# Kernel optimization log

Measured on AMD Instinct MI355X. Metric: run time of the kernel, lower is better.

Reference implementation:

```python
import jax, jax.numpy as jnp
import numpy as np

DEPTH = 4
N_MOLS = 2000
ATOMS_PER_MOL = 50
N_ATOMS = N_MOLS * ATOMS_PER_MOL + 1   # +1 zero-padding row (chemprop convention)
N_BONDS = 200001                        # +1 zero-padding row
MAX_NB = 6
ATOM_FDIM, BOND_FDIM, HIDDEN = 133, 147, 300


def setup_inputs() -> dict:
    key = jax.random.key(0)
    ks = jax.random.split(key, 12)
    f_atoms = jax.random.uniform(ks[0], (N_ATOMS, ATOM_FDIM), jnp.float32).at[0].set(0.0)
    f_bonds = jax.random.uniform(ks[1], (N_BONDS, BOND_FDIM), jnp.float32).at[0].set(0.0)
    w_atoms = jax.random.uniform(ks[2], (N_ATOMS,), jnp.float32) + 0.5
    w_bonds = (jax.random.uniform(ks[3], (N_BONDS,), jnp.float32) + 0.5).at[0].set(0.0)
    a2b = jax.random.randint(ks[4], (N_ATOMS, MAX_NB), 0, N_BONDS, jnp.int32)
    b2a = jax.random.randint(ks[5], (N_BONDS,), 0, N_ATOMS, jnp.int32)
    b2revb = jax.random.randint(ks[6], (N_BONDS,), 0, N_BONDS, jnp.int32)
    # segment id per atom; padding atom 0 -> dummy segment N_MOLS (dropped)
    mol_id = jnp.concatenate([jnp.array([N_MOLS], jnp.int32),
                              jnp.repeat(jnp.arange(N_MOLS, dtype=jnp.int32), ATOMS_PER_MOL)])
    degree_of_polym = jax.random.uniform(ks[7], (N_MOLS,), jnp.float32) + 0.5
    s = 0.05
    W_i = jax.random.normal(ks[8], (BOND_FDIM, HIDDEN), jnp.float32) * s
    W_h = jax.random.normal(ks[9], (HIDDEN, HIDDEN), jnp.float32) * s
    W_o = jax.random.normal(ks[10], (ATOM_FDIM + HIDDEN, HIDDEN), jnp.float32) * s
    b_o = jnp.zeros((HIDDEN,), jnp.float32)
    return dict(f_atoms=f_atoms, f_bonds=f_bonds, w_atoms=w_atoms, w_bonds=w_bonds,
                degree_of_polym=degree_of_polym, W_i=W_i, W_h=W_h, W_o=W_o, b_o=b_o,
                a2b=a2b, b2a=b2a, b2revb=b2revb, mol_id=mol_id)


def reference(f_atoms, f_bonds, w_atoms, w_bonds, degree_of_polym,
              W_i, W_h, W_o, b_o, a2b, b2a, b2revb, mol_id):
    # bond-message MPNN (atom_messages=False, undirected=False, ReLU, dropout=0 eval)
    inp = f_bonds @ W_i                                   # [n_bonds, H], no bias
    message = jax.nn.relu(inp)
    for _ in range(DEPTH - 1):
        # gather incoming directed-bond messages per atom and weight them
        nei_msg = message[a2b] * w_bonds[a2b][..., None]  # [n_atoms, max_nb, H]
        a_message = nei_msg.sum(axis=1)                   # [n_atoms, H]
        # subtract reverse message (weighted)
        message = a_message[b2a] - message[b2revb] * w_bonds[:, None]
        message = jax.nn.relu(inp + message @ W_h)
    # final atom aggregation
    nei_msg = message[a2b] * w_bonds[a2b][..., None]
    a_message = nei_msg.sum(axis=1)                       # [n_atoms, H]
    a_input = jnp.concatenate([f_atoms, a_message], axis=1)
    atom_hiddens = jax.nn.relu(a_input @ W_o + b_o)       # [n_atoms, H]
    # per-molecule weighted mean readout, scaled by degree of polymerization
    weighted = w_atoms[:, None] * atom_hiddens
    sums = jax.ops.segment_sum(weighted, mol_id, num_segments=N_MOLS + 1)[:N_MOLS]
    wsum = jax.ops.segment_sum(w_atoms, mol_id, num_segments=N_MOLS + 1)[:N_MOLS]
    mol_vecs = degree_of_polym[:, None] * (sums / wsum[:, None])
    return mol_vecs
```

## Files before the change

### kernel.cpp

```cpp
#include <hip/hip_runtime.h>

#define N_MOLS  2000
#define APM     50
#define N_ATOMS 100001
#define N_BONDS 200001
#define MAX_NB  6
#define AF      133
#define BF      147
#define H       300

#define SB    320
#define SF    160
#define MB_P  200192
#define MA_P  100096
#define SWH   320
#define SWI   160
#define SWO   480

typedef _Float16 f16x8 __attribute__((ext_vector_type(8)));
typedef _Float16 f16x4 __attribute__((ext_vector_type(4)));
typedef float    f32x4 __attribute__((ext_vector_type(4)));
typedef float    f32x2 __attribute__((ext_vector_type(2)));

__device__ inline void fp8x8_dec(const uint2 u, float* f) {
    const f32x2 d0 = __builtin_amdgcn_cvt_pk_f32_fp8(u.x, false);
    const f32x2 d1 = __builtin_amdgcn_cvt_pk_f32_fp8(u.x, true);
    const f32x2 d2 = __builtin_amdgcn_cvt_pk_f32_fp8(u.y, false);
    const f32x2 d3 = __builtin_amdgcn_cvt_pk_f32_fp8(u.y, true);
    f[0]=d0[0]; f[1]=d0[1]; f[2]=d1[0]; f[3]=d1[1];
    f[4]=d2[0]; f[5]=d2[1]; f[6]=d3[0]; f[7]=d3[1];
}
__device__ inline uint2 fp8x8_enc(const float* f) {
    int w0 = __builtin_amdgcn_cvt_pk_fp8_f32(f[0], f[1], 0, false);
    w0 = __builtin_amdgcn_cvt_pk_fp8_f32(f[2], f[3], w0, true);
    int w1 = __builtin_amdgcn_cvt_pk_fp8_f32(f[4], f[5], 0, false);
    w1 = __builtin_amdgcn_cvt_pk_fp8_f32(f[6], f[7], w1, true);
    uint2 r; r.x = (unsigned)w0; r.y = (unsigned)w1; return r;
}

__global__ void cast_fb_kernel(const float* __restrict__ src, _Float16* __restrict__ dst) {
    unsigned i = blockIdx.x * blockDim.x + threadIdx.x;
    if (i >= (unsigned)MB_P * SF) return;
    unsigned m = i / SF, k = i % SF;
    dst[i] = (_Float16)((m < N_BONDS && k < BF) ? src[(size_t)m * BF + k] : 0.f);
}
__global__ void cast_fa_kernel(const float* __restrict__ src, _Float16* __restrict__ dst) {
    unsigned i = blockIdx.x * blockDim.x + threadIdx.x;
    if (i >= (unsigned)MA_P * SF) return;
    unsigned m = i / SF, k = i % SF;
    dst[i] = (_Float16)((m < N_ATOMS && k < AF) ? src[(size_t)m * AF + k] : 0.f);
}
__global__ void cast_wh_kernel(const float* __restrict__ W, _Float16* __restrict__ Wt) {
    int i = blockIdx.x * blockDim.x + threadIdx.x;
    if (i >= 320 * SWH) return;
    const int e = i & 7, quad = (i >> 3) & 3, r16 = (i >> 5) & 15;
    const int rest = i >> 9, ctg = rest % 20, kc = rest / 20;
    const int n = ctg * 16 + r16, k = kc * 32 + quad * 8 + e;
    Wt[i] = (_Float16)((n < H && k < H) ? W[k * H + n] : 0.f);
}
__global__ void cast_wi_kernel(const float* __restrict__ W, _Float16* __restrict__ Wt) {
    int i = blockIdx.x * blockDim.x + threadIdx.x;
    if (i >= 320 * SWI) return;
    const int e = i & 7, quad = (i >> 3) & 3, r16 = (i >> 5) & 15;
    const int rest = i >> 9, ctg = rest % 20, kc = rest / 20;
    const int n = ctg * 16 + r16, k = kc * 32 + quad * 8 + e;
    Wt[i] = (_Float16)((n < H && k < BF) ? W[k * H + n] : 0.f);
}
__global__ void cast_wo_kernel(const float* __restrict__ W, _Float16* __restrict__ Wt) {
    int i = blockIdx.x * blockDim.x + threadIdx.x;
    if (i >= 320 * SWO) return;
    const int e = i & 7, quad = (i >> 3) & 3, r16 = (i >> 5) & 15;
    const int rest = i >> 9, ctg = rest % 20, kc = rest / 20;
    const int n = ctg * 16 + r16, k = kc * 32 + quad * 8 + e;
    float v = 0.f;
    if (n < H) {
        if (k < 320) { if (k < H) v = W[(AF + k) * H + n]; }
        else         { int rr = k - 320; if (rr < AF) v = W[rr * H + n]; }
    }
    Wt[i] = (_Float16)v;
}

template<int NCHUNK, int MODE>
__global__ __launch_bounds__(256, 2) void dgemm_kernel(
    const _Float16* __restrict__ A1, const _Float16* __restrict__ A2,
    const unsigned char* __restrict__ A8,
    const _Float16* __restrict__ Wt, const float* __restrict__ bias,
    _Float16* __restrict__ out16, unsigned char* __restrict__ out8)
{
    __shared__ __align__(16) _Float16 stage[32 * 324];

    const int tid  = threadIdx.x;
    const int lane = tid & 63, wave = tid >> 6;
    const int r16  = lane & 15, quad = lane >> 4;
    const int rowhalf = wave >> 1, colhalf = wave & 1;
    const int row0 = blockIdx.x * 128 + rowhalf * 64;
    const int colb = colhalf * 160;

    f32x4 acc[4][10];
    #pragma unroll
    for (int s = 0; s < 4; ++s)
        #pragma unroll
        for (int ct = 0; ct < 10; ++ct) acc[s][ct] = f32x4{0.f, 0.f, 0.f, 0.f};

    const _Float16* wb = Wt + (size_t)colhalf * 10 * 512 + (r16 * 4 + quad) * 8;

    #pragma unroll
    for (int kc = 0; kc < NCHUNK; ++kc) {
        f16x8 a[4];
        if constexpr (MODE == 4 || MODE == 5) {
            #pragma unroll
            for (int s = 0; s < 4; ++s) {
                const uint2 u = *(const uint2*)(A8 + (size_t)(row0 + s * 16 + r16) * 320 + kc * 32 + quad * 8);
                float f[8];
                fp8x8_dec(u, f);
                #pragma unroll
                for (int j = 0; j < 8; ++j) {
                    float v = f[j];
                    if (MODE == 4) v = v > 0.f ? v : 0.f;
                    a[s][j] = (_Float16)v;
                }
            }
        } else {
            const _Float16* ap; int kl, sa;
            if (MODE == 2 && kc >= 10) { ap = A2; kl = kc - 10; sa = SF; }
            else                       { ap = A1; kl = kc; sa = (MODE == 0 ? SF : SB); }
            #pragma unroll
            for (int s = 0; s < 4; ++s)
                a[s] = *(const f16x8*)(ap + (size_t)(row0 + s * 16 + r16) * sa + kl * 32 + quad * 8);
        }
        #pragma unroll
        for (int ct = 0; ct < 10; ++ct) {
            const f16x8 b = *(const f16x8*)(wb + (size_t)(kc * 20 + ct) * 512);
            #pragma unroll
            for (int s = 0; s < 4; ++s)
                acc[s][ct] = __builtin_amdgcn_mfma_f32_16x16x32_f16(a[s], b, acc[s][ct], 0, 0, 0);
        }
    }

    #pragma unroll
    for (int p = 0; p < 4; ++p) {
        if ((p >> 1) == rowhalf) {
            const int sb0 = (p & 1) * 2;
            #pragma unroll
            for (int s2 = 0; s2 < 2; ++s2) {
                const int s = sb0 + s2;
                #pragma unroll
                for (int ct = 0; ct < 10; ++ct) {
                    const int col = colb + ct * 16 + r16;
                    const float bv = (MODE == 2 && col < H) ? bias[col] : 0.f;
                    const int lr = s2 * 16 + quad * 4;
                    #pragma unroll
                    for (int e = 0; e < 4; ++e)
                        stage[(lr + e) * 324 + col] = (_Float16)(acc[s][ct][e] + bv);
                }
            }
        }
        __syncthreads();
        #pragma unroll
        for (int i = 0; i < 5; ++i) {
            const int c = tid + i * 256;
            const int row = c / 40, colc = (c % 40) * 8;
            const _Float16* sp = stage + row * 324 + colc;
            const f16x4 vlo = *(const f16x4*)(sp);
            const f16x4 vhi = *(const f16x4*)(sp + 4);
            f16x8 v;
            #pragma unroll
            for (int j = 0; j < 4; ++j) { v[j] = vlo[j]; v[j + 4] = vhi[j]; }
            const size_t off = (size_t)(blockIdx.x * 128 + p * 32 + row) * SB + colc;
            if (MODE == 0) {
                float f[8];
                #pragma unroll
                for (int j = 0; j < 8; ++j) f[j] = (float)v[j];
                *(uint2*)(out8 + off) = fp8x8_enc(f);
            } else {
                if (MODE == 2) {
                    #pragma unroll
                    for (int j = 0; j < 8; ++j)
                        v[j] = (v[j] > (_Float16)0) ? v[j] : (_Float16)0;
                }
                *(f16x8*)(out16 + off) = v;
            }
        }
        if (p < 3) __syncthreads();
    }
}

__global__ __launch_bounds__(256, 8) void aggregate_kernel(
    const _Float16* __restrict__ src,
    const int* __restrict__ a2b,
    const float* __restrict__ w_bonds,
    _Float16* __restrict__ dst)
{
    const int lane = threadIdx.x & 63;
    const int a = blockIdx.x * 4 + (threadIdx.x >> 6);
    if (a >= N_ATOMS || lane >= 40) return;
    const int h0 = lane * 8;
    float acc[8] = {0, 0, 0, 0, 0, 0, 0, 0};
    #pragma unroll
    for (int k = 0; k < MAX_NB; ++k) {
        const int b = a2b[a * MAX_NB + k];
        const float w = w_bonds[b];
        const f16x8 m = *(const f16x8*)(src + (size_t)b * SB + h0);
        #pragma unroll
        for (int j = 0; j < 8; ++j) acc[j] += w * (float)m[j];
    }
    f16x8 o;
    #pragma unroll
    for (int j = 0; j < 8; ++j) o[j] = (_Float16)acc[j];
    *(f16x8*)(dst + (size_t)a * SB + h0) = o;
}

__global__ __launch_bounds__(256, 8) void aggregate8_kernel(
    const unsigned char* __restrict__ src,
    const int* __restrict__ a2b,
    const float* __restrict__ w_bonds,
    _Float16* __restrict__ dst)
{
    const int lane = threadIdx.x & 63;
    const int a = blockIdx.x * 4 + (threadIdx.x >> 6);
    if (a >= N_ATOMS || lane >= 40) return;
    const int h0 = lane * 8;
    float acc[8] = {0, 0, 0, 0, 0, 0, 0, 0};
    #pragma unroll
    for (int k = 0; k < MAX_NB; ++k) {
        const int b = a2b[a * MAX_NB + k];
        const float w = w_bonds[b];
        const uint2 u = *(const uint2*)(src + (size_t)b * 320 + h0);
        float f[8];
        fp8x8_dec(u, f);
        #pragma unroll
        for (int j = 0; j < 8; ++j) acc[j] += w * f[j];
    }
    f16x8 o;
    #pragma unroll
    for (int j = 0; j < 8; ++j) o[j] = (_Float16)acc[j];
    *(f16x8*)(dst + (size_t)a * SB + h0) = o;
}

__global__ __launch_bounds__(256, 8) void update_kernel(
    const unsigned char* __restrict__ inp8,
    const _Float16* __restrict__ hm,
    const _Float16* __restrict__ hb,
    const int* __restrict__ b2a,
    const int* __restrict__ b2revb,
    const float* __restrict__ w_bonds,
    unsigned char* __restrict__ msg8)
{
    const int lane = threadIdx.x & 63;
    const int b = blockIdx.x * 4 + (threadIdx.x >> 6);
    if (b >= MB_P || lane >= 40) return;
    const bool real = b < N_BONDS;
    const int bc = real ? b : 0;
    const int a  = b2a[bc];
    const int rb = b2revb[bc];
    const float w = w_bonds[bc];
    const int h0 = lane * 8;
    const uint2 i8  = *(const uint2*)(inp8 + (size_t)b * 320 + h0);
    const f16x8 hmv = *(const f16x8*)(hm + (size_t)a  * SB + h0);
    const f16x8 hbv = *(const f16x8*)(hb + (size_t)rb * SB + h0);
    float inpf[8];
    fp8x8_dec(i8, inpf);
    float o[8];
    #pragma unroll
    for (int j = 0; j < 8; ++j) {
        const float v = inpf[j] + (float)hmv[j] - w * (float)hbv[j];
        o[j] = (real && v > 0.f) ? v : 0.f;
    }
    *(uint2*)(msg8 + (size_t)b * 320 + h0) = fp8x8_enc(o);
}

__global__ __launch_bounds__(256, 8) void readout_kernel(
    const _Float16* __restrict__ ah,
    const float* __restrict__ w_atoms,
    const float* __restrict__ dop,
    float* __restrict__ out)
{
    const int lane = threadIdx.x & 63;
    const int m = blockIdx.x * 4 + (threadIdx.x >> 6);
    if (m >= N_MOLS || lane >= 40) return;
    const int h0 = lane * 8;
    const int a0 = 1 + m * APM;
    float acc[8] = {0, 0, 0, 0, 0, 0, 0, 0};
    float wsum = 0.f;
    for (int i = 0; i < APM; ++i) {
        const float w = w_atoms[a0 + i];
        wsum += w;
        const f16x8 v = *(const f16x8*)(ah + (size_t)(a0 + i) * SB + h0);
        #pragma unroll
        for (int j = 0; j < 8; ++j) acc[j] += w * (float)v[j];
    }
    const float s = dop[m] / wsum;
    #pragma unroll
    for (int j = 0; j < 8; ++j) {
        const int h = h0 + j;
        if (h < H) out[(size_t)m * H + h] = s * acc[j];
    }
}

extern "C" void kernel_launch(void* const* d_in, const int* in_sizes, int n_in,
                              void* d_out, int out_size, void* d_ws, size_t ws_size,
                              hipStream_t stream) {
    const float* f_atoms = (const float*)d_in[0];
    const float* f_bonds = (const float*)d_in[1];
    const float* w_atoms = (const float*)d_in[2];
    const float* w_bonds = (const float*)d_in[3];
    const float* dop     = (const float*)d_in[4];
    const float* W_i     = (const float*)d_in[5];
    const float* W_h     = (const float*)d_in[6];
    const float* W_o     = (const float*)d_in[7];
    const float* b_o     = (const float*)d_in[8];
    const int* a2b    = (const int*)d_in[9];
    const int* b2a    = (const int*)d_in[10];
    const int* b2revb = (const int*)d_in[11];
    float* out = (float*)d_out;

    char* p = (char*)d_ws;
    auto alloc = [&](size_t bytes) {
        char* q = p;
        p += ((bytes + 64 + 255) / 256) * 256;
        return q;
    };
    unsigned char* inp8 = (unsigned char*)alloc((size_t)MB_P * 320);
    unsigned char* msg8 = (unsigned char*)alloc((size_t)MB_P * 320);
    _Float16* hb   = (_Float16*)alloc((size_t)MB_P * SB * 2);
    _Float16* hm   = (_Float16*)alloc((size_t)MA_P * SB * 2);
    _Float16* Wth  = (_Float16*)alloc((size_t)320 * SWH * 2);
    _Float16* Wti  = (_Float16*)alloc((size_t)320 * SWI * 2);
    _Float16* Wto  = (_Float16*)alloc((size_t)320 * SWO * 2);
    _Float16* fb16 = hb;
    _Float16* fa16 = (_Float16*)inp8;
    _Float16* ah   = hb;

    if ((size_t)(p - (char*)d_ws) > ws_size) {
        hipMemsetAsync(d_out, 0, (size_t)out_size * sizeof(float), stream);
        return;
    }

    {
        unsigned n1 = (unsigned)MB_P * SF;
        cast_fb_kernel<<<(n1 + 255) / 256, 256, 0, stream>>>(f_bonds, fb16);
        cast_wh_kernel<<<(320 * SWH + 255) / 256, 256, 0, stream>>>(W_h, Wth);
        cast_wi_kernel<<<(320 * SWI + 255) / 256, 256, 0, stream>>>(W_i, Wti);
        cast_wo_kernel<<<(320 * SWO + 255) / 256, 256, 0, stream>>>(W_o, Wto);
    }

    const int gB = MB_P / 128;
    const int gA = MA_P / 128;
    const int aggGrid = (N_ATOMS + 3) / 4;
    const int updGrid = MB_P / 4;

    dgemm_kernel<5, 0><<<gB, 256, 0, stream>>>(fb16, nullptr, nullptr, Wti, nullptr, nullptr, inp8);
    dgemm_kernel<10, 4><<<gB, 256, 0, stream>>>(nullptr, nullptr, inp8, Wth, nullptr, hb, nullptr);
    aggregate_kernel<<<aggGrid, 256, 0, stream>>>(hb, a2b, w_bonds, hm);
    update_kernel<<<updGrid, 256, 0, stream>>>(inp8, hm, hb, b2a, b2revb, w_bonds, msg8);
    dgemm_kernel<10, 5><<<gB, 256, 0, stream>>>(nullptr, nullptr, msg8, Wth, nullptr, hb, nullptr);
    aggregate_kernel<<<aggGrid, 256, 0, stream>>>(hb, a2b, w_bonds, hm);
    update_kernel<<<updGrid, 256, 0, stream>>>(inp8, hm, hb, b2a, b2revb, w_bonds, msg8);
    dgemm_kernel<10, 5><<<gB, 256, 0, stream>>>(nullptr, nullptr, msg8, Wth, nullptr, hb, nullptr);
    aggregate_kernel<<<aggGrid, 256, 0, stream>>>(hb, a2b, w_bonds, hm);
    update_kernel<<<updGrid, 256, 0, stream>>>(inp8, hm, hb, b2a, b2revb, w_bonds, msg8);
    aggregate8_kernel<<<aggGrid, 256, 0, stream>>>(msg8, a2b, w_bonds, hm);
    {
        unsigned n2 = (unsigned)MA_P * SF;
        cast_fa_kernel<<<(n2 + 255) / 256, 256, 0, stream>>>(f_atoms, fa16);
    }
    dgemm_kernel<15, 2><<<gA, 256, 0, stream>>>(hm, fa16, nullptr, Wto, b_o, ah, nullptr);
    readout_kernel<<<(N_MOLS + 3) / 4, 256, 0, stream>>>(ah, w_atoms, dop, out);
}
```

Measured before the change: 1.137 ms.

## Stage fp8 A tiles through LDS and pack elementwise threads densely

Adds a dedicated fp8-input GEMM kernel that copies the block's 128x320 fp8 A tile into shared memory with coalesced 16-byte loads, then decodes from LDS, replacing strided 8-byte global loads per lane. The aggregate and update kernels switch from one wave per row with 24 idle lanes to flat indexing over row×40 chunks, so every lane does work. The generic GEMM now always applies ReLU on fp16 output, since only MODE 2 still uses it. The cost is extra LDS use (about 42KB per block) that may limit occupancy, plus div/mod by 40 in the elementwise kernels.

```diff
diff --git a/kernel.cpp b/kernel.cpp
--- a/kernel.cpp
+++ b/kernel.cpp
@@ -83,7 +83,6 @@
 template<int NCHUNK, int MODE>
 __global__ __launch_bounds__(256, 2) void dgemm_kernel(
     const _Float16* __restrict__ A1, const _Float16* __restrict__ A2,
-    const unsigned char* __restrict__ A8,
     const _Float16* __restrict__ Wt, const float* __restrict__ bias,
     _Float16* __restrict__ out16, unsigned char* __restrict__ out8)
 {
@@ -106,28 +105,13 @@
 
     #pragma unroll
     for (int kc = 0; kc < NCHUNK; ++kc) {
+        const _Float16* ap; int kl, sa;
+        if (MODE == 2 && kc >= 10) { ap = A2; kl = kc - 10; sa = SF; }
+        else                       { ap = A1; kl = kc; sa = (MODE == 0 ? SF : SB); }
         f16x8 a[4];
-        if constexpr (MODE == 4 || MODE == 5) {
-            #pragma unroll
-            for (int s = 0; s < 4; ++s) {
-                const uint2 u = *(const uint2*)(A8 + (size_t)(row0 + s * 16 + r16) * 320 + kc * 32 + quad * 8);
-                float f[8];
-                fp8x8_dec(u, f);
-                #pragma unroll
-                for (int j = 0; j < 8; ++j) {
-                    float v = f[j];
-                    if (MODE == 4) v = v > 0.f ? v : 0.f;
-                    a[s][j] = (_Float16)v;
-                }
-            }
-        } else {
-            const _Float16* ap; int kl, sa;
-            if (MODE == 2 && kc >= 10) { ap = A2; kl = kc - 10; sa = SF; }
-            else                       { ap = A1; kl = kc; sa = (MODE == 0 ? SF : SB); }
-            #pragma unroll
-            for (int s = 0; s < 4; ++s)
-                a[s] = *(const f16x8*)(ap + (size_t)(row0 + s * 16 + r16) * sa + kl * 32 + quad * 8);
-        }
+        #pragma unroll
+        for (int s = 0; s < 4; ++s)
+            a[s] = *(const f16x8*)(ap + (size_t)(row0 + s * 16 + r16) * sa + kl * 32 + quad * 8);
         #pragma unroll
         for (int ct = 0; ct < 10; ++ct) {
             const f16x8 b = *(const f16x8*)(wb + (size_t)(kc * 20 + ct) * 512);
@@ -173,13 +157,103 @@
                 for (int j = 0; j < 8; ++j) f[j] = (float)v[j];
                 *(uint2*)(out8 + off) = fp8x8_enc(f);
             } else {
-                if (MODE == 2) {
-                    #pragma unroll
-                    for (int j = 0; j < 8; ++j)
-                        v[j] = (v[j] > (_Float16)0) ? v[j] : (_Float16)0;
-                }
+                #pragma unroll
+                for (int j = 0; j < 8; ++j)
+                    v[j] = (v[j] > (_Float16)0) ? v[j] : (_Float16)0;
                 *(f16x8*)(out16 + off) = v;
             }
+        }
+        if (p < 3) __syncthreads();
+    }
+}
+
+template<int RELU>
+__global__ __launch_bounds__(256, 2) void dgemm8_kernel(
+    const unsigned char* __restrict__ A8,
+    const _Float16* __restrict__ Wt,
+    _Float16* __restrict__ out16)
+{
+    __shared__ __align__(16) unsigned char Als[128 * 328];
+    __shared__ __align__(16) _Float16 stage[32 * 324];
+
+    const int tid  = threadIdx.x;
+    const int lane = tid & 63, wave = tid >> 6;
+    const int r16  = lane & 15, quad = lane >> 4;
+    const int rowhalf = wave >> 1, colhalf = wave & 1;
+    const int colb = colhalf * 160;
+    const size_t gbase = (size_t)blockIdx.x * 128 * 320;
+
+    #pragma unroll
+    for (int i = 0; i < 10; ++i) {
+        const int idx = tid + i * 256;
+        const int row = idx / 20, col = idx % 20;
+        const uint4 v = *(const uint4*)(A8 + gbase + (size_t)idx * 16);
+        *(uint4*)(&Als[row * 328 + col * 16]) = v;
+    }
+    __syncthreads();
+
+    f32x4 acc[4][10];
+    #pragma unroll
+    for (int s = 0; s < 4; ++s)
+        #pragma unroll
+        for (int ct = 0; ct < 10; ++ct) acc[s][ct] = f32x4{0.f, 0.f, 0.f, 0.f};
+
+    const _Float16* wb = Wt + (size_t)colhalf * 10 * 512 + (r16 * 4 + quad) * 8;
+
+    #pragma unroll
+    for (int kc = 0; kc < 10; ++kc) {
+        f16x8 a[4];
+        #pragma unroll
+        for (int s = 0; s < 4; ++s) {
+            const int lrow = rowhalf * 64 + s * 16 + r16;
+            const uint2 u = *(const uint2*)(&Als[lrow * 328 + kc * 32 + quad * 8]);
+            float f[8];
+            fp8x8_dec(u, f);
+            #pragma unroll
+            for (int j = 0; j < 8; ++j) {
+                float v = f[j];
+                if (RELU) v = v > 0.f ? v : 0.f;
+                a[s][j] = (_Float16)v;
+            }
+        }
+        #pragma unroll
+        for (int ct = 0; ct < 10; ++ct) {
+            const f16x8 b = *(const f16x8*)(wb + (size_t)(kc * 20 + ct) * 512);
+            #pragma unroll
+            for (int s = 0; s < 4; ++s)
+                acc[s][ct] = __builtin_amdgcn_mfma_f32_16x16x32_f16(a[s], b, acc[s][ct], 0, 0, 0);
+        }
+    }
+
+    #pragma unroll
+    for (int p = 0; p < 4; ++p) {
+        if ((p >> 1) == rowhalf) {
+            const int sb0 = (p & 1) * 2;
+            #pragma unroll
+            for (int s2 = 0; s2 < 2; ++s2) {
+                const int s = sb0 + s2;
+                #pragma unroll
+                for (int ct = 0; ct < 10; ++ct) {
+                    const int col = colb + ct * 16 + r16;
+                    const int lr = s2 * 16 + quad * 4;
+                    #pragma unroll
+                    for (int e = 0; e < 4; ++e)
+                        stage[(lr + e) * 324 + col] = (_Float16)acc[s][ct][e];
+                }
+            }
+        }
+        __syncthreads();
+        #pragma unroll
+        for (int i = 0; i < 5; ++i) {
+            const int c = tid + i * 256;
+            const int row = c / 40, colc = (c % 40) * 8;
+            const _Float16* sp = stage + row * 324 + colc;
+            const f16x4 vlo = *(const f16x4*)(sp);
+            const f16x4 vhi = *(const f16x4*)(sp + 4);
+            f16x8 v;
+            #pragma unroll
+            for (int j = 0; j < 4; ++j) { v[j] = vlo[j]; v[j + 4] = vhi[j]; }
+            *(f16x8*)(out16 + (size_t)(blockIdx.x * 128 + p * 32 + row) * SB + colc) = v;
         }
         if (p < 3) __syncthreads();
     }
@@ -191,10 +265,10 @@
     const float* __restrict__ w_bonds,
     _Float16* __restrict__ dst)
 {
-    const int lane = threadIdx.x & 63;
-    const int a = blockIdx.x * 4 + (threadIdx.x >> 6);
-    if (a >= N_ATOMS || lane >= 40) return;
-    const int h0 = lane * 8;
+    const unsigned idx = blockIdx.x * 256 + threadIdx.x;
+    if (idx >= (unsigned)N_ATOMS * 40) return;
+    const int a = idx / 40, c = idx % 40;
+    const int h0 = c * 8;
     float acc[8] = {0, 0, 0, 0, 0, 0, 0, 0};
     #pragma unroll
     for (int k = 0; k < MAX_NB; ++k) {
@@ -216,10 +290,10 @@
     const float* __restrict__ w_bonds,
     _Float16* __restrict__ dst)
 {
-    const int lane = threadIdx.x & 63;
-    const int a = blockIdx.x * 4 + (threadIdx.x >> 6);
-    if (a >= N_ATOMS || lane >= 40) return;
-    const int h0 = lane * 8;
+    const unsigned idx = blockIdx.x * 256 + threadIdx.x;
+    if (idx >= (unsigned)N_ATOMS * 40) return;
+    const int a = idx / 40, c = idx % 40;
+    const int h0 = c * 8;
     float acc[8] = {0, 0, 0, 0, 0, 0, 0, 0};
     #pragma unroll
     for (int k = 0; k < MAX_NB; ++k) {
@@ -246,15 +320,15 @@
     const float* __restrict__ w_bonds,
     unsigned char* __restrict__ msg8)
 {
-    const int lane = threadIdx.x & 63;
-    const int b = blockIdx.x * 4 + (threadIdx.x >> 6);
-    if (b >= MB_P || lane >= 40) return;
+    const unsigned idx = blockIdx.x * 256 + threadIdx.x;
+    if (idx >= (unsigned)MB_P * 40) return;
+    const int b = idx / 40, c = idx % 40;
     const bool real = b < N_BONDS;
     const int bc = real ? b : 0;
     const int a  = b2a[bc];
     const int rb = b2revb[bc];
     const float w = w_bonds[bc];
-    const int h0 = lane * 8;
+    const int h0 = c * 8;
     const uint2 i8  = *(const uint2*)(inp8 + (size_t)b * 320 + h0);
     const f16x8 hmv = *(const f16x8*)(hm + (size_t)a  * SB + h0);
     const f16x8 hbv = *(const f16x8*)(hb + (size_t)rb * SB + h0);
@@ -346,17 +420,17 @@
 
     const int gB = MB_P / 128;
     const int gA = MA_P / 128;
-    const int aggGrid = (N_ATOMS + 3) / 4;
-    const int updGrid = MB_P / 4;
-
-    dgemm_kernel<5, 0><<<gB, 256, 0, stream>>>(fb16, nullptr, nullptr, Wti, nullptr, nullptr, inp8);
-    dgemm_kernel<10, 4><<<gB, 256, 0, stream>>>(nullptr, nullptr, inp8, Wth, nullptr, hb, nullptr);
+    const int aggGrid = ((unsigned)N_ATOMS * 40 + 255) / 256;
+    const int updGrid = ((unsigned)MB_P * 40) / 256;
+
+    dgemm_kernel<5, 0><<<gB, 256, 0, stream>>>(fb16, nullptr, Wti, nullptr, nullptr, inp8);
+    dgemm8_kernel<1><<<gB, 256, 0, stream>>>(inp8, Wth, hb);
     aggregate_kernel<<<aggGrid, 256, 0, stream>>>(hb, a2b, w_bonds, hm);
     update_kernel<<<updGrid, 256, 0, stream>>>(inp8, hm, hb, b2a, b2revb, w_bonds, msg8);
-    dgemm_kernel<10, 5><<<gB, 256, 0, stream>>>(nullptr, nullptr, msg8, Wth, nullptr, hb, nullptr);
+    dgemm8_kernel<0><<<gB, 256, 0, stream>>>(msg8, Wth, hb);
     aggregate_kernel<<<aggGrid, 256, 0, stream>>>(hb, a2b, w_bonds, hm);
     update_kernel<<<updGrid, 256, 0, stream>>>(inp8, hm, hb, b2a, b2revb, w_bonds, msg8);
-    dgemm_kernel<10, 5><<<gB, 256, 0, stream>>>(nullptr, nullptr, msg8, Wth, nullptr, hb, nullptr);
+    dgemm8_kernel<0><<<gB, 256, 0, stream>>>(msg8, Wth, hb);
     aggregate_kernel<<<aggGrid, 256, 0, stream>>>(hb, a2b, w_bonds, hm);
     update_kernel<<<updGrid, 256, 0, stream>>>(inp8, hm, hb, b2a, b2revb, w_bonds, msg8);
     aggregate8_kernel<<<aggGrid, 256, 0, stream>>>(msg8, a2b, w_bonds, hm);
@@ -364,6 +438,6 @@
         unsigned n2 = (unsigned)MA_P * SF;
         cast_fa_kernel<<<(n2 + 255) / 256, 256, 0, stream>>>(f_atoms, fa16);
     }
-    dgemm_kernel<15, 2><<<gA, 256, 0, stream>>>(hm, fa16, nullptr, Wto, b_o, ah, nullptr);
+    dgemm_kernel<15, 2><<<gA, 256, 0, stream>>>(hm, fa16, Wto, b_o, ah, nullptr);
     readout_kernel<<<(N_MOLS + 3) / 4, 256, 0, stream>>>(ah, w_atoms, dop, out);
 }
```

Result: faster. 1.104 ms (-2.9%).
